# Kernel optimization log

Hardware: AMD Instinct MI355X
Metric: run time of the kernel (lower is better)

The kernel has to match this reference:

```python
import jax, jax.numpy as jnp
import numpy as np

N_NODES = 100000
IN_FEAT, HID, OUT_FEAT, GRID = 128, 64, 40, 8
N_EDGES = 1600000


def spmm(row, col, w, x):
    # out[i] = sum_{e: row[e]==i} w[e] * x[col[e]]
    return jax.ops.segment_sum(w[:, None] * x[col], row, num_segments=N_NODES)


def kan_layer(x, coeff):
    # coeff: [2, out, in, grid]; Fourier KAN: y[b,j] = sum_{i,k} cos(k x_bi) C0[j,i,k] + sin(k x_bi) C1[j,i,k]
    grid = coeff.shape[-1]
    k = jnp.arange(1, grid + 1, dtype=x.dtype)  # [G]
    ang = x[:, :, None] * k  # [N, in, G]
    y = jnp.einsum('bik,jik->bj', jnp.cos(ang), coeff[0])
    y = y + jnp.einsum('bik,jik->bj', jnp.sin(ang), coeff[1])
    return y


def setup_inputs() -> dict:
    key = jax.random.key(0)
    ks = jax.random.split(key, 8)
    scale = 1.0 / (np.sqrt(HID) * np.sqrt(GRID))
    return {
        'x': jax.random.normal(ks[0], (N_NODES, IN_FEAT), dtype=jnp.float32),
        'edge_row': jax.random.randint(ks[1], (N_EDGES,), 0, N_NODES),
        'edge_col': jax.random.randint(ks[2], (N_EDGES,), 0, N_NODES),
        'edge_weight': jax.random.uniform(ks[3], (N_EDGES,), dtype=jnp.float32),
        'W_in': jax.random.normal(ks[4], (IN_FEAT, HID), dtype=jnp.float32) / np.sqrt(IN_FEAT),
        'b_in': jnp.zeros((HID,), dtype=jnp.float32),
        'coeffs1': jax.random.normal(ks[5], (2, HID, HID, GRID), dtype=jnp.float32) * scale,
        'coeffs2': jax.random.normal(ks[6], (2, HID, HID, GRID), dtype=jnp.float32) * scale,
        'W_out': jax.random.normal(ks[7], (HID, OUT_FEAT), dtype=jnp.float32) / np.sqrt(HID),
    }


def reference(x, edge_row, edge_col, edge_weight, W_in, b_in, coeffs1, coeffs2, W_out):
    h = x @ W_in + b_in                                  # lin_in
    h = kan_layer(spmm(edge_row, edge_col, edge_weight, h), coeffs1)
    h = kan_layer(spmm(edge_row, edge_col, edge_weight, h), coeffs2)
    out = h @ W_out                                      # final bias-free linear
    return jax.nn.log_softmax(out, axis=-1)
```

## Files before the change

### kernel.cpp

```cpp
#include <hip/hip_runtime.h>
#include <hip/hip_bf16.h>
#include <string.h>


#define N_NODES 100000
#define IN_FEAT 128
#define HID 64
#define OUT_FEAT 40
#define NGRID 8
#define N_EDGES 1600000
#define NELEM (N_NODES * HID)

#define NB 98
#define CAP 18432
#define BCHUNK 4096
#define BIN_BLOCKS ((N_EDGES + BCHUNK - 1) / BCHUNK)

using short8 = __attribute__((ext_vector_type(8))) short;
using floatx4 = __attribute__((ext_vector_type(4))) float;
using uintx4 = __attribute__((ext_vector_type(4))) unsigned;

#define GLOAD_LDS16(gp, lp)                                                   \
  __builtin_amdgcn_global_load_lds(                                           \
      (const __attribute__((address_space(1))) unsigned*)(gp),                \
      (__attribute__((address_space(3))) unsigned*)(lp), 16, 0, 0)

__device__ __forceinline__ unsigned pack_bf16x2(float c, float s) {
  unsigned uc = __float_as_uint(c);
  unsigned us = __float_as_uint(s);
  uc += 0x7fffu + ((uc >> 16) & 1u);
  us += 0x7fffu + ((us >> 16) & 1u);
  return (uc >> 16) | (us & 0xffff0000u);
}

__device__ __forceinline__ unsigned cvtpk_bf16x2(float c, float s) {
  __hip_bfloat162 p = __float22bfloat162_rn(make_float2(c, s));
  unsigned r;
  memcpy(&r, &p, 4);
  return r;
}

__global__ __launch_bounds__(256) void lin_in_kernel(
    const float* __restrict__ x, const float* __restrict__ W,
    const float* __restrict__ b, float* __restrict__ h) {
  __shared__ __align__(16) float xs[16 * IN_FEAT];
  int t = threadIdx.x;
  int nb = blockIdx.x;
  const float4* xsrc = (const float4*)(x + (size_t)nb * 16 * IN_FEAT);
  float4* xd = (float4*)xs;
  xd[t] = xsrc[t];
  xd[t + 256] = xsrc[t + 256];
  __syncthreads();
  int lane = t & 63, wv = t >> 6;
  float bj = b[lane];
  float a0 = bj, a1 = bj, a2 = bj, a3 = bj;
  const float* xr = xs + wv * 4 * IN_FEAT;
  const float* Wj = W + lane;
#pragma unroll 4
  for (int i4 = 0; i4 < 32; i4++) {
    float4 x0 = *(const float4*)(xr + 0 * IN_FEAT + i4 * 4);
    float4 x1 = *(const float4*)(xr + 1 * IN_FEAT + i4 * 4);
    float4 x2 = *(const float4*)(xr + 2 * IN_FEAT + i4 * 4);
    float4 x3 = *(const float4*)(xr + 3 * IN_FEAT + i4 * 4);
    float w0 = Wj[(i4 * 4 + 0) * HID];
    float w1 = Wj[(i4 * 4 + 1) * HID];
    float w2 = Wj[(i4 * 4 + 2) * HID];
    float w3 = Wj[(i4 * 4 + 3) * HID];
    a0 = fmaf(x0.x, w0, a0); a0 = fmaf(x0.y, w1, a0); a0 = fmaf(x0.z, w2, a0); a0 = fmaf(x0.w, w3, a0);
    a1 = fmaf(x1.x, w0, a1); a1 = fmaf(x1.y, w1, a1); a1 = fmaf(x1.z, w2, a1); a1 = fmaf(x1.w, w3, a1);
    a2 = fmaf(x2.x, w0, a2); a2 = fmaf(x2.y, w1, a2); a2 = fmaf(x2.z, w2, a2); a2 = fmaf(x2.w, w3, a2);
    a3 = fmaf(x3.x, w0, a3); a3 = fmaf(x3.y, w1, a3); a3 = fmaf(x3.z, w2, a3); a3 = fmaf(x3.w, w3, a3);
  }
  size_t nbase = (size_t)nb * 16 + wv * 4;
  h[(nbase + 0) * HID + lane] = a0;
  h[(nbase + 1) * HID + lane] = a1;
  h[(nbase + 2) * HID + lane] = a2;
  h[(nbase + 3) * HID + lane] = a3;
}

__global__ __launch_bounds__(128) void binit_kernel(int* __restrict__ btail) {
  int t = threadIdx.x;
  if (t < NB) btail[t] = t * CAP;
}

__global__ __launch_bounds__(256) void bin_kernel(
    const int* __restrict__ row, const int* __restrict__ col,
    const float* __restrict__ w, int* __restrict__ btail,
    uint2* __restrict__ pack1) {
  __shared__ __align__(16) uint2 stage[BCHUNK];
  __shared__ int bcnt[NB];
  __shared__ int lbase[NB];
  __shared__ int gbase[NB];
  __shared__ int lcur[NB];
  __shared__ int sc[128];
  int t = threadIdx.x;
  int e0 = blockIdx.x * BCHUNK;
  if (t < NB) bcnt[t] = 0;
  __syncthreads();
  int rloc[16];
#pragma unroll
  for (int q = 0; q < 16; q++) {
    int e = e0 + q * 256 + t;
    int r = (e < N_EDGES) ? row[e] : -1;
    rloc[q] = r;
    if (r >= 0) atomicAdd(&bcnt[r >> 10], 1);
  }
  __syncthreads();
  int c = (t < NB) ? bcnt[t] : 0;
  if (t < 128) sc[t] = c;
  __syncthreads();
  int v = c;
#pragma unroll
  for (int off = 1; off < 128; off <<= 1) {
    int add = (t >= off && t < 128) ? sc[t - off] : 0;
    __syncthreads();
    if (t < 128) sc[t] = v = v + add;
    __syncthreads();
  }
  if (t < NB) {
    lbase[t] = v - c;
    lcur[t] = v - c;
    gbase[t] = atomicAdd(&btail[t], c);
  }
  __syncthreads();
#pragma unroll
  for (int q = 0; q < 16; q++) {
    int e = e0 + q * 256 + t;
    int r = rloc[q];
    if (r >= 0) {
      int p = atomicAdd(&lcur[r >> 10], 1);
      unsigned key = ((unsigned)(r & 1023) << 17) | (unsigned)col[e];
      stage[p] = make_uint2(key, __float_as_uint(w[e]));
    }
  }
  __syncthreads();
  int wv = t >> 6, lane = t & 63;
  for (int b = wv; b < NB; b += 4) {
    int len = bcnt[b], src = lbase[b];
    uint2* dst = pack1 + (size_t)gbase[b];
    for (int i = lane; i < len; i += 64)
      dst[i] = stage[src + i];
  }
}

__global__ __launch_bounds__(256) void bucket_finalize_kernel(
    const int* __restrict__ btail, const uint2* __restrict__ pack1,
    int* __restrict__ rowptr, uint2* __restrict__ pack2) {
  __shared__ int rcnt[1024];
  __shared__ int sc[256];
  __shared__ int binfo[2];
  int b = blockIdx.x, t = threadIdx.x;
  if (t < NB) sc[t] = btail[t] - t * CAP;
  rcnt[t] = 0; rcnt[t + 256] = 0; rcnt[t + 512] = 0; rcnt[t + 768] = 0;
  __syncthreads();
  if (t == 0) {
    int base = 0;
    for (int i = 0; i < b; i++) base += sc[i];
    binfo[0] = base;
    binfo[1] = sc[b];
  }
  __syncthreads();
  int base = binfo[0], len = binfo[1];
  const uint2* rec = pack1 + (size_t)b * CAP;
  for (int i = t; i < len; i += 256)
    atomicAdd(&rcnt[rec[i].x >> 17], 1);
  __syncthreads();
  int c0 = rcnt[4 * t], c1 = rcnt[4 * t + 1], c2 = rcnt[4 * t + 2], c3 = rcnt[4 * t + 3];
  int s4 = c0 + c1 + c2 + c3;
  sc[t] = s4;
  __syncthreads();
  int v = s4;
#pragma unroll
  for (int off = 1; off < 256; off <<= 1) {
    int add = (t >= off) ? sc[t - off] : 0;
    __syncthreads();
    sc[t] = v = v + add;
    __syncthreads();
  }
  int excl = v - s4;
  int p0 = base + excl;
  int p1 = p0 + c0, p2 = p1 + c1, p3 = p2 + c2;
  int r0 = (b << 10) + 4 * t;
  if (r0 + 0 < N_NODES) rowptr[r0 + 0] = p0;
  if (r0 + 1 < N_NODES) rowptr[r0 + 1] = p1;
  if (r0 + 2 < N_NODES) rowptr[r0 + 2] = p2;
  if (r0 + 3 < N_NODES) rowptr[r0 + 3] = p3;
  rcnt[4 * t] = p0; rcnt[4 * t + 1] = p1; rcnt[4 * t + 2] = p2; rcnt[4 * t + 3] = p3;
  __syncthreads();
  for (int i = t; i < len; i += 256) {
    uint2 p = rec[i];
    int pos = atomicAdd(&rcnt[p.x >> 17], 1);
    pack2[pos] = make_uint2(p.x & 0x1FFFFu, p.y);
  }
  if (b == NB - 1 && t == 0) rowptr[N_NODES] = N_EDGES;
}

__global__ __launch_bounds__(256) void repack_kernel(
    const float* __restrict__ coeffs, unsigned* __restrict__ Brep) {
  int idx = blockIdx.x * 256 + threadIdx.x;
  int ch = idx >> 13;
  int rem = idx & 8191;
  int blk = rem >> 8;
  int jt = blk >> 3, ks = blk & 7;
  int rem2 = rem & 255;
  int ls = rem2 >> 2;
  int quad = ls >> 4, m_n = ls & 15;
  int jj = rem2 & 3;
  int j = jt * 16 + m_n;
  int r = ks >> 1, km1 = ((ks & 1) << 2) | jj;
  int i = ch * 16 + quad * 4 + r;
  int ws = i * 8 + km1;
  float c0 = coeffs[(size_t)j * 512 + ws];
  float c1 = coeffs[32768 + (size_t)j * 512 + ws];
  Brep[idx] = pack_bf16x2(c0, c1);
}

template <int DO_FINAL>
__global__ __launch_bounds__(256, 4) void fused_spmm_kan_kernel(
    const int* __restrict__ rowptr, const uint2* __restrict__ pack,
    const float* __restrict__ hin, const unsigned* __restrict__ Brep,
    float* __restrict__ outp, const float* __restrict__ Wout) {
  __shared__ __align__(16) unsigned Bs[2][2048];
  __shared__ __align__(16) float s_tile[64 * 64];
  int t = threadIdx.x;
  int lane = t & 63, wv = t >> 6;
  int nb = blockIdx.x;
  const char* Gb = (const char*)Brep;

#pragma unroll
  for (int i = 0; i < 2; i++) {
    int c = wv + 4 * i;
    GLOAD_LDS16(Gb + c * 1024 + lane * 16, (char*)&Bs[0][0] + c * 1024);
  }

  {
    int rpi = nb * 64 + wv * 16 + lane;
    int rp = 0;
    if (lane < 17) rp = rowptr[rpi < N_NODES ? rpi : N_NODES];
    int slot = lane >> 4, f4 = lane & 15;
    const float4* h4 = (const float4*)hin;
    const unsigned long long* packq = (const unsigned long long*)pack;
    for (int i = 0; i < 16; i++) {
      int beg = __shfl(rp, i), end = __shfl(rp, i + 1);
      float4 v = make_float4(0.f, 0.f, 0.f, 0.f);
      for (int e = beg; e < end; e += 16) {
        int i0 = e + slot, i1 = i0 + 4, i2 = i0 + 8, i3 = i0 + 12;
        int c0 = i0 < end ? i0 : end - 1;
        int c1 = i1 < end ? i1 : end - 1;
        int c2 = i2 < end ? i2 : end - 1;
        int c3 = i3 < end ? i3 : end - 1;
        unsigned long long p0 = __builtin_nontemporal_load(packq + c0);
        unsigned long long p1 = __builtin_nontemporal_load(packq + c1);
        unsigned long long p2 = __builtin_nontemporal_load(packq + c2);
        unsigned long long p3 = __builtin_nontemporal_load(packq + c3);
        float4 h0 = h4[(size_t)(unsigned)p0 * 16 + f4];
        float4 h1 = h4[(size_t)(unsigned)p1 * 16 + f4];
        float4 h2 = h4[(size_t)(unsigned)p2 * 16 + f4];
        float4 h3 = h4[(size_t)(unsigned)p3 * 16 + f4];
        float w0 = (i0 < end) ? __uint_as_float((unsigned)(p0 >> 32)) : 0.f;
        float w1 = (i1 < end) ? __uint_as_float((unsigned)(p1 >> 32)) : 0.f;
        float w2 = (i2 < end) ? __uint_as_float((unsigned)(p2 >> 32)) : 0.f;
        float w3 = (i3 < end) ? __uint_as_float((unsigned)(p3 >> 32)) : 0.f;
        v.x = fmaf(w0, h0.x, v.x); v.y = fmaf(w0, h0.y, v.y);
        v.z = fmaf(w0, h0.z, v.z); v.w = fmaf(w0, h0.w, v.w);
        v.x = fmaf(w1, h1.x, v.x); v.y = fmaf(w1, h1.y, v.y);
        v.z = fmaf(w1, h1.z, v.z); v.w = fmaf(w1, h1.w, v.w);
        v.x = fmaf(w2, h2.x, v.x); v.y = fmaf(w2, h2.y, v.y);
        v.z = fmaf(w2, h2.z, v.z); v.w = fmaf(w2, h2.w, v.w);
        v.x = fmaf(w3, h3.x, v.x); v.y = fmaf(w3, h3.y, v.y);
        v.z = fmaf(w3, h3.z, v.z); v.w = fmaf(w3, h3.w, v.w);
      }
#pragma unroll
      for (int off = 16; off < 64; off <<= 1) {
        v.x += __shfl_xor(v.x, off);
        v.y += __shfl_xor(v.y, off);
        v.z += __shfl_xor(v.z, off);
        v.w += __shfl_xor(v.w, off);
      }
      if (slot == 0)
        *(float4*)&s_tile[(wv * 16 + i) * 64 + f4 * 4] = v;
    }
  }
  __syncthreads();

  int m_n = lane & 15, quad = lane >> 4;
  int node_sub = wv * 16 + m_n;
  float4 sv[4];
#pragma unroll
  for (int ch = 0; ch < 4; ch++)
    sv[ch] = *(const float4*)&s_tile[node_sub * 64 + ch * 16 + quad * 4];

  floatx4 acc[4];
#pragma unroll
  for (int jt = 0; jt < 4; jt++) acc[jt] = (floatx4){0.f, 0.f, 0.f, 0.f};
  short8 afr[8];

#pragma unroll
  for (int q = 0; q < 16; q++) {
    asm volatile("s_waitcnt vmcnt(0)" ::: "memory");
    __syncthreads();
    if (q < 15) {
      int qq = q + 1;
      const char* gsrc = Gb + (qq >> 2) * 32768 + (qq & 3) * 8192;
      char* ldst = (char*)&Bs[qq & 1][0];
#pragma unroll
      for (int i = 0; i < 2; i++) {
        int c = wv + 4 * i;
        GLOAD_LDS16(gsrc + c * 1024 + lane * 16, ldst + c * 1024);
      }
    }
    if ((q & 3) == 0) {
      int ch = q >> 2;
      float ss[4] = {sv[ch].x, sv[ch].y, sv[ch].z, sv[ch].w};
#pragma unroll
      for (int r = 0; r < 4; r++) {
        float s1, c1;
        __sincosf(ss[r], &s1, &c1);
        float ck = c1, sk = s1;
        unsigned wbuf[8];
#pragma unroll
        for (int km1 = 0; km1 < 8; km1++) {
          wbuf[km1] = cvtpk_bf16x2(ck, sk);
          float cn = fmaf(ck, c1, -sk * s1);
          float sn = fmaf(sk, c1, ck * s1);
          ck = cn; sk = sn;
        }
        uintx4 lo = (uintx4){wbuf[0], wbuf[1], wbuf[2], wbuf[3]};
        uintx4 hi = (uintx4){wbuf[4], wbuf[5], wbuf[6], wbuf[7]};
        memcpy(&afr[2 * r], &lo, 16);
        memcpy(&afr[2 * r + 1], &hi, 16);
      }
    }
    const char* Bb = (const char*)&Bs[q & 1][0];
    int jt = q & 3;
#pragma unroll
    for (int ks = 0; ks < 8; ks++) {
      short8 bf = *reinterpret_cast<const short8*>(Bb + ks * 1024 + lane * 16);
      acc[jt] = __builtin_amdgcn_mfma_f32_16x16x32_bf16(afr[ks], bf, acc[jt], 0, 0, 0);
    }
  }

  if (DO_FINAL == 0) {
#pragma unroll
    for (int jt = 0; jt < 4; jt++) {
#pragma unroll
      for (int reg = 0; reg < 4; reg++) {
        int node = nb * 64 + wv * 16 + quad * 4 + reg;
        if (node < N_NODES)
          outp[(size_t)node * HID + jt * 16 + m_n] = acc[jt][reg];
      }
    }
  } else {
#pragma unroll
    for (int jt = 0; jt < 4; jt++) {
#pragma unroll
      for (int reg = 0; reg < 4; reg++)
        s_tile[(wv * 16 + quad * 4 + reg) * 64 + jt * 16 + m_n] = acc[jt][reg];
    }
    __syncthreads();
    bool jvalid = lane < OUT_FEAT;
    int jc = jvalid ? lane : 0;
    float wl[HID];
#pragma unroll
    for (int i2 = 0; i2 < HID; i2++)
      wl[i2] = Wout[i2 * OUT_FEAT + jc];
    int nwbase = nb * 64 + wv * 16;
    for (int ns = 0; ns < 16; ns += 2) {
      const float* h0p = &s_tile[(wv * 16 + ns) * 64];
      const float* h1p = h0p + 64;
      float d0 = 0.f, d1 = 0.f;
#pragma unroll
      for (int i4 = 0; i4 < 16; i4++) {
        float4 a = *(const float4*)(h0p + i4 * 4);
        float4 b = *(const float4*)(h1p + i4 * 4);
        d0 = fmaf(a.x, wl[i4 * 4 + 0], d0);  d1 = fmaf(b.x, wl[i4 * 4 + 0], d1);
        d0 = fmaf(a.y, wl[i4 * 4 + 1], d0);  d1 = fmaf(b.y, wl[i4 * 4 + 1], d1);
        d0 = fmaf(a.z, wl[i4 * 4 + 2], d0);  d1 = fmaf(b.z, wl[i4 * 4 + 2], d1);
        d0 = fmaf(a.w, wl[i4 * 4 + 3], d0);  d1 = fmaf(b.w, wl[i4 * 4 + 3], d1);
      }
      float m0 = jvalid ? d0 : -1e30f;
      float m1 = jvalid ? d1 : -1e30f;
#pragma unroll
      for (int off = 32; off; off >>= 1) {
        m0 = fmaxf(m0, __shfl_xor(m0, off));
        m1 = fmaxf(m1, __shfl_xor(m1, off));
      }
      float e0 = jvalid ? expf(d0 - m0) : 0.f;
      float e1 = jvalid ? expf(d1 - m1) : 0.f;
      float s0 = e0, s1 = e1;
#pragma unroll
      for (int off = 32; off; off >>= 1) {
        s0 += __shfl_xor(s0, off);
        s1 += __shfl_xor(s1, off);
      }
      float l0 = m0 + logf(s0);
      float l1 = m1 + logf(s1);
      int n0 = nwbase + ns, n1 = n0 + 1;
      if (jvalid) {
        if (n0 < N_NODES) outp[(size_t)n0 * OUT_FEAT + lane] = d0 - l0;
        if (n1 < N_NODES) outp[(size_t)n1 * OUT_FEAT + lane] = d1 - l1;
      }
    }
  }
}

extern "C" void kernel_launch(void* const* d_in, const int* in_sizes, int n_in,
                              void* d_out, int out_size, void* d_ws, size_t ws_size,
                              hipStream_t stream) {
  (void)in_sizes; (void)n_in; (void)out_size; (void)ws_size;
  const float* x    = (const float*)d_in[0];
  const int*   erow = (const int*)d_in[1];
  const int*   ecol = (const int*)d_in[2];
  const float* ew   = (const float*)d_in[3];
  const float* W_in = (const float*)d_in[4];
  const float* b_in = (const float*)d_in[5];
  const float* c1   = (const float*)d_in[6];
  const float* c2   = (const float*)d_in[7];
  const float* Wout = (const float*)d_in[8];
  float* out = (float*)d_out;

  float* h0 = (float*)d_ws;
  float* h1 = h0 + NELEM;

  unsigned* xw     = (unsigned*)(void*)x;
  unsigned* Brep1  = xw;
  unsigned* Brep2  = xw + 32768;
  int*      btail  = (int*)(xw + 65536);
  int*      rowptr = (int*)(xw + 66048);
  uint2*    pack1  = (uint2*)(xw + 262144);
  uint2*    pack2  = (uint2*)(xw + 3932160);

  const int fgrid = (N_NODES + 63) / 64;

  lin_in_kernel<<<N_NODES / 16, 256, 0, stream>>>(x, W_in, b_in, h0);

  repack_kernel<<<128, 256, 0, stream>>>(c1, Brep1);
  repack_kernel<<<128, 256, 0, stream>>>(c2, Brep2);

  binit_kernel<<<1, 128, 0, stream>>>(btail);
  bin_kernel<<<BIN_BLOCKS, 256, 0, stream>>>(erow, ecol, ew, btail, pack1);
  bucket_finalize_kernel<<<NB, 256, 0, stream>>>(btail, pack1, rowptr, pack2);

  fused_spmm_kan_kernel<0><<<fgrid, 256, 0, stream>>>(
      rowptr, pack2, h0, Brep1, h1, nullptr);
  fused_spmm_kan_kernel<1><<<fgrid, 256, 0, stream>>>(
      rowptr, pack2, h1, Brep2, out, Wout);
}
```

Measured before the change: 425.4 us.

## Merge prep kernels and make fused SpMM-KAN kernels persistent with atomic tile queue

The input linear layer, both coefficient repacks and the bucket-tail init are folded into one prep kernel that dispatches on block index. The prep kernel also resets two tile counters. The two fused SpMM+KAN kernels now launch a fixed grid of 1280 blocks, and each block pulls 64-node tiles from an atomic counter until all are done. This cuts launch overhead and evens out load across tiles with uneven row degrees, at the cost of an atomic plus a barrier per tile and a grid size tuned by hand.

```diff
diff --git a/kernel.cpp b/kernel.cpp
--- a/kernel.cpp
+++ b/kernel.cpp
@@ -15,6 +15,8 @@
 #define CAP 18432
 #define BCHUNK 4096
 #define BIN_BLOCKS ((N_EDGES + BCHUNK - 1) / BCHUNK)
+#define NTILES ((N_NODES + 63) / 64)
+#define FGRID 1280
 
 using short8 = __attribute__((ext_vector_type(8))) short;
 using floatx4 = __attribute__((ext_vector_type(4))) float;
@@ -40,47 +42,70 @@
   return r;
 }
 
-__global__ __launch_bounds__(256) void lin_in_kernel(
+__global__ __launch_bounds__(256) void prep_kernel(
     const float* __restrict__ x, const float* __restrict__ W,
-    const float* __restrict__ b, float* __restrict__ h) {
+    const float* __restrict__ b, float* __restrict__ h,
+    const float* __restrict__ c1, const float* __restrict__ c2,
+    unsigned* __restrict__ Brep1, unsigned* __restrict__ Brep2,
+    int* __restrict__ btail, int* __restrict__ ctrs) {
   __shared__ __align__(16) float xs[16 * IN_FEAT];
   int t = threadIdx.x;
   int nb = blockIdx.x;
-  const float4* xsrc = (const float4*)(x + (size_t)nb * 16 * IN_FEAT);
-  float4* xd = (float4*)xs;
-  xd[t] = xsrc[t];
-  xd[t + 256] = xsrc[t + 256];
-  __syncthreads();
-  int lane = t & 63, wv = t >> 6;
-  float bj = b[lane];
-  float a0 = bj, a1 = bj, a2 = bj, a3 = bj;
-  const float* xr = xs + wv * 4 * IN_FEAT;
-  const float* Wj = W + lane;
+  if (nb < 6250) {
+    const float4* xsrc = (const float4*)(x + (size_t)nb * 16 * IN_FEAT);
+    float4* xd = (float4*)xs;
+    xd[t] = xsrc[t];
+    xd[t + 256] = xsrc[t + 256];
+    __syncthreads();
+    int lane = t & 63, wv = t >> 6;
+    float bj = b[lane];
+    float a0 = bj, a1 = bj, a2 = bj, a3 = bj;
+    const float* xr = xs + wv * 4 * IN_FEAT;
+    const float* Wj = W + lane;
 #pragma unroll 4
-  for (int i4 = 0; i4 < 32; i4++) {
-    float4 x0 = *(const float4*)(xr + 0 * IN_FEAT + i4 * 4);
-    float4 x1 = *(const float4*)(xr + 1 * IN_FEAT + i4 * 4);
-    float4 x2 = *(const float4*)(xr + 2 * IN_FEAT + i4 * 4);
-    float4 x3 = *(const float4*)(xr + 3 * IN_FEAT + i4 * 4);
-    float w0 = Wj[(i4 * 4 + 0) * HID];
-    float w1 = Wj[(i4 * 4 + 1) * HID];
-    float w2 = Wj[(i4 * 4 + 2) * HID];
-    float w3 = Wj[(i4 * 4 + 3) * HID];
-    a0 = fmaf(x0.x, w0, a0); a0 = fmaf(x0.y, w1, a0); a0 = fmaf(x0.z, w2, a0); a0 = fmaf(x0.w, w3, a0);
-    a1 = fmaf(x1.x, w0, a1); a1 = fmaf(x1.y, w1, a1); a1 = fmaf(x1.z, w2, a1); a1 = fmaf(x1.w, w3, a1);
-    a2 = fmaf(x2.x, w0, a2); a2 = fmaf(x2.y, w1, a2); a2 = fmaf(x2.z, w2, a2); a2 = fmaf(x2.w, w3, a2);
-    a3 = fmaf(x3.x, w0, a3); a3 = fmaf(x3.y, w1, a3); a3 = fmaf(x3.z, w2, a3); a3 = fmaf(x3.w, w3, a3);
-  }
-  size_t nbase = (size_t)nb * 16 + wv * 4;
-  h[(nbase + 0) * HID + lane] = a0;
-  h[(nbase + 1) * HID + lane] = a1;
-  h[(nbase + 2) * HID + lane] = a2;
-  h[(nbase + 3) * HID + lane] = a3;
-}
-
-__global__ __launch_bounds__(128) void binit_kernel(int* __restrict__ btail) {
-  int t = threadIdx.x;
-  if (t < NB) btail[t] = t * CAP;
+    for (int i4 = 0; i4 < 32; i4++) {
+      float4 x0 = *(const float4*)(xr + 0 * IN_FEAT + i4 * 4);
+      float4 x1 = *(const float4*)(xr + 1 * IN_FEAT + i4 * 4);
+      float4 x2 = *(const float4*)(xr + 2 * IN_FEAT + i4 * 4);
+      float4 x3 = *(const float4*)(xr + 3 * IN_FEAT + i4 * 4);
+      float w0 = Wj[(i4 * 4 + 0) * HID];
+      float w1 = Wj[(i4 * 4 + 1) * HID];
+      float w2 = Wj[(i4 * 4 + 2) * HID];
+      float w3 = Wj[(i4 * 4 + 3) * HID];
+      a0 = fmaf(x0.x, w0, a0); a0 = fmaf(x0.y, w1, a0); a0 = fmaf(x0.z, w2, a0); a0 = fmaf(x0.w, w3, a0);
+      a1 = fmaf(x1.x, w0, a1); a1 = fmaf(x1.y, w1, a1); a1 = fmaf(x1.z, w2, a1); a1 = fmaf(x1.w, w3, a1);
+      a2 = fmaf(x2.x, w0, a2); a2 = fmaf(x2.y, w1, a2); a2 = fmaf(x2.z, w2, a2); a2 = fmaf(x2.w, w3, a2);
+      a3 = fmaf(x3.x, w0, a3); a3 = fmaf(x3.y, w1, a3); a3 = fmaf(x3.z, w2, a3); a3 = fmaf(x3.w, w3, a3);
+    }
+    size_t nbase = (size_t)nb * 16 + wv * 4;
+    h[(nbase + 0) * HID + lane] = a0;
+    h[(nbase + 1) * HID + lane] = a1;
+    h[(nbase + 2) * HID + lane] = a2;
+    h[(nbase + 3) * HID + lane] = a3;
+  } else if (nb < 6506) {
+    int rb = nb - 6250;
+    const float* coeffs = (rb < 128) ? c1 : c2;
+    unsigned* Brep = (rb < 128) ? Brep1 : Brep2;
+    int idx = (rb & 127) * 256 + t;
+    int ch = idx >> 13;
+    int rem = idx & 8191;
+    int blk = rem >> 8;
+    int jt = blk >> 3, ks = blk & 7;
+    int rem2 = rem & 255;
+    int ls = rem2 >> 2;
+    int quad = ls >> 4, m_n = ls & 15;
+    int jj = rem2 & 3;
+    int j = jt * 16 + m_n;
+    int r = ks >> 1, km1 = ((ks & 1) << 2) | jj;
+    int i = ch * 16 + quad * 4 + r;
+    int ws = i * 8 + km1;
+    float cc0 = coeffs[(size_t)j * 512 + ws];
+    float cc1 = coeffs[32768 + (size_t)j * 512 + ws];
+    Brep[idx] = pack_bf16x2(cc0, cc1);
+  } else {
+    if (t < NB) btail[t] = t * CAP;
+    if (t == 128) { ctrs[0] = 0; ctrs[1] = 0; }
+  }
 }
 
 __global__ __launch_bounds__(256) void bin_kernel(
@@ -195,210 +220,197 @@
   if (b == NB - 1 && t == 0) rowptr[N_NODES] = N_EDGES;
 }
 
-__global__ __launch_bounds__(256) void repack_kernel(
-    const float* __restrict__ coeffs, unsigned* __restrict__ Brep) {
-  int idx = blockIdx.x * 256 + threadIdx.x;
-  int ch = idx >> 13;
-  int rem = idx & 8191;
-  int blk = rem >> 8;
-  int jt = blk >> 3, ks = blk & 7;
-  int rem2 = rem & 255;
-  int ls = rem2 >> 2;
-  int quad = ls >> 4, m_n = ls & 15;
-  int jj = rem2 & 3;
-  int j = jt * 16 + m_n;
-  int r = ks >> 1, km1 = ((ks & 1) << 2) | jj;
-  int i = ch * 16 + quad * 4 + r;
-  int ws = i * 8 + km1;
-  float c0 = coeffs[(size_t)j * 512 + ws];
-  float c1 = coeffs[32768 + (size_t)j * 512 + ws];
-  Brep[idx] = pack_bf16x2(c0, c1);
-}
-
 template <int DO_FINAL>
 __global__ __launch_bounds__(256, 4) void fused_spmm_kan_kernel(
     const int* __restrict__ rowptr, const uint2* __restrict__ pack,
     const float* __restrict__ hin, const unsigned* __restrict__ Brep,
-    float* __restrict__ outp, const float* __restrict__ Wout) {
+    float* __restrict__ outp, const float* __restrict__ Wout,
+    int* __restrict__ ctr) {
   __shared__ __align__(16) unsigned Bs[2][2048];
   __shared__ __align__(16) float s_tile[64 * 64];
+  __shared__ int tile_sm;
   int t = threadIdx.x;
   int lane = t & 63, wv = t >> 6;
-  int nb = blockIdx.x;
   const char* Gb = (const char*)Brep;
-
-#pragma unroll
-  for (int i = 0; i < 2; i++) {
-    int c = wv + 4 * i;
-    GLOAD_LDS16(Gb + c * 1024 + lane * 16, (char*)&Bs[0][0] + c * 1024);
-  }
-
-  {
-    int rpi = nb * 64 + wv * 16 + lane;
-    int rp = 0;
-    if (lane < 17) rp = rowptr[rpi < N_NODES ? rpi : N_NODES];
-    int slot = lane >> 4, f4 = lane & 15;
-    const float4* h4 = (const float4*)hin;
-    const unsigned long long* packq = (const unsigned long long*)pack;
-    for (int i = 0; i < 16; i++) {
-      int beg = __shfl(rp, i), end = __shfl(rp, i + 1);
-      float4 v = make_float4(0.f, 0.f, 0.f, 0.f);
-      for (int e = beg; e < end; e += 16) {
-        int i0 = e + slot, i1 = i0 + 4, i2 = i0 + 8, i3 = i0 + 12;
-        int c0 = i0 < end ? i0 : end - 1;
-        int c1 = i1 < end ? i1 : end - 1;
-        int c2 = i2 < end ? i2 : end - 1;
-        int c3 = i3 < end ? i3 : end - 1;
-        unsigned long long p0 = __builtin_nontemporal_load(packq + c0);
-        unsigned long long p1 = __builtin_nontemporal_load(packq + c1);
-        unsigned long long p2 = __builtin_nontemporal_load(packq + c2);
-        unsigned long long p3 = __builtin_nontemporal_load(packq + c3);
-        float4 h0 = h4[(size_t)(unsigned)p0 * 16 + f4];
-        float4 h1 = h4[(size_t)(unsigned)p1 * 16 + f4];
-        float4 h2 = h4[(size_t)(unsigned)p2 * 16 + f4];
-        float4 h3 = h4[(size_t)(unsigned)p3 * 16 + f4];
-        float w0 = (i0 < end) ? __uint_as_float((unsigned)(p0 >> 32)) : 0.f;
-        float w1 = (i1 < end) ? __uint_as_float((unsigned)(p1 >> 32)) : 0.f;
-        float w2 = (i2 < end) ? __uint_as_float((unsigned)(p2 >> 32)) : 0.f;
-        float w3 = (i3 < end) ? __uint_as_float((unsigned)(p3 >> 32)) : 0.f;
-        v.x = fmaf(w0, h0.x, v.x); v.y = fmaf(w0, h0.y, v.y);
-        v.z = fmaf(w0, h0.z, v.z); v.w = fmaf(w0, h0.w, v.w);
-        v.x = fmaf(w1, h1.x, v.x); v.y = fmaf(w1, h1.y, v.y);
-        v.z = fmaf(w1, h1.z, v.z); v.w = fmaf(w1, h1.w, v.w);
-        v.x = fmaf(w2, h2.x, v.x); v.y = fmaf(w2, h2.y, v.y);
-        v.z = fmaf(w2, h2.z, v.z); v.w = fmaf(w2, h2.w, v.w);
-        v.x = fmaf(w3, h3.x, v.x); v.y = fmaf(w3, h3.y, v.y);
-        v.z = fmaf(w3, h3.z, v.z); v.w = fmaf(w3, h3.w, v.w);
-      }
-#pragma unroll
-      for (int off = 16; off < 64; off <<= 1) {
-        v.x += __shfl_xor(v.x, off);
-        v.y += __shfl_xor(v.y, off);
-        v.z += __shfl_xor(v.z, off);
-        v.w += __shfl_xor(v.w, off);
-      }
-      if (slot == 0)
-        *(float4*)&s_tile[(wv * 16 + i) * 64 + f4 * 4] = v;
-    }
-  }
-  __syncthreads();
-
   int m_n = lane & 15, quad = lane >> 4;
-  int node_sub = wv * 16 + m_n;
-  float4 sv[4];
-#pragma unroll
-  for (int ch = 0; ch < 4; ch++)
-    sv[ch] = *(const float4*)&s_tile[node_sub * 64 + ch * 16 + quad * 4];
-
-  floatx4 acc[4];
-#pragma unroll
-  for (int jt = 0; jt < 4; jt++) acc[jt] = (floatx4){0.f, 0.f, 0.f, 0.f};
-  short8 afr[8];
-
-#pragma unroll
-  for (int q = 0; q < 16; q++) {
-    asm volatile("s_waitcnt vmcnt(0)" ::: "memory");
-    __syncthreads();
-    if (q < 15) {
-      int qq = q + 1;
-      const char* gsrc = Gb + (qq >> 2) * 32768 + (qq & 3) * 8192;
-      char* ldst = (char*)&Bs[qq & 1][0];
-#pragma unroll
-      for (int i = 0; i < 2; i++) {
-        int c = wv + 4 * i;
-        GLOAD_LDS16(gsrc + c * 1024 + lane * 16, ldst + c * 1024);
-      }
-    }
-    if ((q & 3) == 0) {
-      int ch = q >> 2;
-      float ss[4] = {sv[ch].x, sv[ch].y, sv[ch].z, sv[ch].w};
-#pragma unroll
-      for (int r = 0; r < 4; r++) {
-        float s1, c1;
-        __sincosf(ss[r], &s1, &c1);
-        float ck = c1, sk = s1;
-        unsigned wbuf[8];
-#pragma unroll
-        for (int km1 = 0; km1 < 8; km1++) {
-          wbuf[km1] = cvtpk_bf16x2(ck, sk);
-          float cn = fmaf(ck, c1, -sk * s1);
-          float sn = fmaf(sk, c1, ck * s1);
-          ck = cn; sk = sn;
-        }
-        uintx4 lo = (uintx4){wbuf[0], wbuf[1], wbuf[2], wbuf[3]};
-        uintx4 hi = (uintx4){wbuf[4], wbuf[5], wbuf[6], wbuf[7]};
-        memcpy(&afr[2 * r], &lo, 16);
-        memcpy(&afr[2 * r + 1], &hi, 16);
-      }
-    }
-    const char* Bb = (const char*)&Bs[q & 1][0];
-    int jt = q & 3;
-#pragma unroll
-    for (int ks = 0; ks < 8; ks++) {
-      short8 bf = *reinterpret_cast<const short8*>(Bb + ks * 1024 + lane * 16);
-      acc[jt] = __builtin_amdgcn_mfma_f32_16x16x32_bf16(afr[ks], bf, acc[jt], 0, 0, 0);
-    }
-  }
-
-  if (DO_FINAL == 0) {
-#pragma unroll
-    for (int jt = 0; jt < 4; jt++) {
-#pragma unroll
-      for (int reg = 0; reg < 4; reg++) {
-        int node = nb * 64 + wv * 16 + quad * 4 + reg;
-        if (node < N_NODES)
-          outp[(size_t)node * HID + jt * 16 + m_n] = acc[jt][reg];
-      }
-    }
-  } else {
-#pragma unroll
-    for (int jt = 0; jt < 4; jt++) {
-#pragma unroll
-      for (int reg = 0; reg < 4; reg++)
-        s_tile[(wv * 16 + quad * 4 + reg) * 64 + jt * 16 + m_n] = acc[jt][reg];
-    }
-    __syncthreads();
-    bool jvalid = lane < OUT_FEAT;
-    int jc = jvalid ? lane : 0;
-    float wl[HID];
-#pragma unroll
-    for (int i2 = 0; i2 < HID; i2++)
-      wl[i2] = Wout[i2 * OUT_FEAT + jc];
-    int nwbase = nb * 64 + wv * 16;
-    for (int ns = 0; ns < 16; ns += 2) {
-      const float* h0p = &s_tile[(wv * 16 + ns) * 64];
-      const float* h1p = h0p + 64;
-      float d0 = 0.f, d1 = 0.f;
-#pragma unroll
-      for (int i4 = 0; i4 < 16; i4++) {
-        float4 a = *(const float4*)(h0p + i4 * 4);
-        float4 b = *(const float4*)(h1p + i4 * 4);
-        d0 = fmaf(a.x, wl[i4 * 4 + 0], d0);  d1 = fmaf(b.x, wl[i4 * 4 + 0], d1);
-        d0 = fmaf(a.y, wl[i4 * 4 + 1], d0);  d1 = fmaf(b.y, wl[i4 * 4 + 1], d1);
-        d0 = fmaf(a.z, wl[i4 * 4 + 2], d0);  d1 = fmaf(b.z, wl[i4 * 4 + 2], d1);
-        d0 = fmaf(a.w, wl[i4 * 4 + 3], d0);  d1 = fmaf(b.w, wl[i4 * 4 + 3], d1);
-      }
-      float m0 = jvalid ? d0 : -1e30f;
-      float m1 = jvalid ? d1 : -1e30f;
-#pragma unroll
-      for (int off = 32; off; off >>= 1) {
-        m0 = fmaxf(m0, __shfl_xor(m0, off));
-        m1 = fmaxf(m1, __shfl_xor(m1, off));
-      }
-      float e0 = jvalid ? expf(d0 - m0) : 0.f;
-      float e1 = jvalid ? expf(d1 - m1) : 0.f;
-      float s0 = e0, s1 = e1;
-#pragma unroll
-      for (int off = 32; off; off >>= 1) {
-        s0 += __shfl_xor(s0, off);
-        s1 += __shfl_xor(s1, off);
-      }
-      float l0 = m0 + logf(s0);
-      float l1 = m1 + logf(s1);
-      int n0 = nwbase + ns, n1 = n0 + 1;
-      if (jvalid) {
-        if (n0 < N_NODES) outp[(size_t)n0 * OUT_FEAT + lane] = d0 - l0;
-        if (n1 < N_NODES) outp[(size_t)n1 * OUT_FEAT + lane] = d1 - l1;
+
+  while (true) {
+    if (t == 0) tile_sm = atomicAdd(ctr, 1);
+    __syncthreads();
+    int nb = tile_sm;
+    if (nb >= NTILES) break;
+
+#pragma unroll
+    for (int i = 0; i < 2; i++) {
+      int c = wv + 4 * i;
+      GLOAD_LDS16(Gb + c * 1024 + lane * 16, (char*)&Bs[0][0] + c * 1024);
+    }
+
+    {
+      int rpi = nb * 64 + wv * 16 + lane;
+      int rp = 0;
+      if (lane < 17) rp = rowptr[rpi < N_NODES ? rpi : N_NODES];
+      int slot = lane >> 4, f4 = lane & 15;
+      const float4* h4 = (const float4*)hin;
+      const unsigned long long* packq = (const unsigned long long*)pack;
+      for (int i = 0; i < 16; i++) {
+        int beg = __shfl(rp, i), end = __shfl(rp, i + 1);
+        float4 v = make_float4(0.f, 0.f, 0.f, 0.f);
+        for (int e = beg; e < end; e += 16) {
+          int i0 = e + slot, i1 = i0 + 4, i2 = i0 + 8, i3 = i0 + 12;
+          int c0 = i0 < end ? i0 : end - 1;
+          int c1 = i1 < end ? i1 : end - 1;
+          int c2 = i2 < end ? i2 : end - 1;
+          int c3 = i3 < end ? i3 : end - 1;
+          unsigned long long p0 = __builtin_nontemporal_load(packq + c0);
+          unsigned long long p1 = __builtin_nontemporal_load(packq + c1);
+          unsigned long long p2 = __builtin_nontemporal_load(packq + c2);
+          unsigned long long p3 = __builtin_nontemporal_load(packq + c3);
+          float4 h0 = h4[(size_t)(unsigned)p0 * 16 + f4];
+          float4 h1 = h4[(size_t)(unsigned)p1 * 16 + f4];
+          float4 h2 = h4[(size_t)(unsigned)p2 * 16 + f4];
+          float4 h3 = h4[(size_t)(unsigned)p3 * 16 + f4];
+          float w0 = (i0 < end) ? __uint_as_float((unsigned)(p0 >> 32)) : 0.f;
+          float w1 = (i1 < end) ? __uint_as_float((unsigned)(p1 >> 32)) : 0.f;
+          float w2 = (i2 < end) ? __uint_as_float((unsigned)(p2 >> 32)) : 0.f;
+          float w3 = (i3 < end) ? __uint_as_float((unsigned)(p3 >> 32)) : 0.f;
+          v.x = fmaf(w0, h0.x, v.x); v.y = fmaf(w0, h0.y, v.y);
+          v.z = fmaf(w0, h0.z, v.z); v.w = fmaf(w0, h0.w, v.w);
+          v.x = fmaf(w1, h1.x, v.x); v.y = fmaf(w1, h1.y, v.y);
+          v.z = fmaf(w1, h1.z, v.z); v.w = fmaf(w1, h1.w, v.w);
+          v.x = fmaf(w2, h2.x, v.x); v.y = fmaf(w2, h2.y, v.y);
+          v.z = fmaf(w2, h2.z, v.z); v.w = fmaf(w2, h2.w, v.w);
+          v.x = fmaf(w3, h3.x, v.x); v.y = fmaf(w3, h3.y, v.y);
+          v.z = fmaf(w3, h3.z, v.z); v.w = fmaf(w3, h3.w, v.w);
+        }
+#pragma unroll
+        for (int off = 16; off < 64; off <<= 1) {
+          v.x += __shfl_xor(v.x, off);
+          v.y += __shfl_xor(v.y, off);
+          v.z += __shfl_xor(v.z, off);
+          v.w += __shfl_xor(v.w, off);
+        }
+        if (slot == 0)
+          *(float4*)&s_tile[(wv * 16 + i) * 64 + f4 * 4] = v;
+      }
+    }
+    __syncthreads();
+
+    float4 sv[4];
+#pragma unroll
+    for (int ch = 0; ch < 4; ch++)
+      sv[ch] = *(const float4*)&s_tile[(wv * 16 + m_n) * 64 + ch * 16 + quad * 4];
+
+    floatx4 acc[4];
+#pragma unroll
+    for (int jt = 0; jt < 4; jt++) acc[jt] = (floatx4){0.f, 0.f, 0.f, 0.f};
+    short8 afr[8];
+
+#pragma unroll
+    for (int q = 0; q < 16; q++) {
+      asm volatile("s_waitcnt vmcnt(0)" ::: "memory");
+      __syncthreads();
+      if (q < 15) {
+        int qq = q + 1;
+        const char* gsrc = Gb + (qq >> 2) * 32768 + (qq & 3) * 8192;
+        char* ldst = (char*)&Bs[qq & 1][0];
+#pragma unroll
+        for (int i = 0; i < 2; i++) {
+          int c = wv + 4 * i;
+          GLOAD_LDS16(gsrc + c * 1024 + lane * 16, ldst + c * 1024);
+        }
+      }
+      if ((q & 3) == 0) {
+        int ch = q >> 2;
+        float ss[4] = {sv[ch].x, sv[ch].y, sv[ch].z, sv[ch].w};
+#pragma unroll
+        for (int r = 0; r < 4; r++) {
+          float s1, c1;
+          __sincosf(ss[r], &s1, &c1);
+          float ck = c1, sk = s1;
+          unsigned wbuf[8];
+#pragma unroll
+          for (int km1 = 0; km1 < 8; km1++) {
+            wbuf[km1] = cvtpk_bf16x2(ck, sk);
+            float cn = fmaf(ck, c1, -sk * s1);
+            float sn = fmaf(sk, c1, ck * s1);
+            ck = cn; sk = sn;
+          }
+          uintx4 lo = (uintx4){wbuf[0], wbuf[1], wbuf[2], wbuf[3]};
+          uintx4 hi = (uintx4){wbuf[4], wbuf[5], wbuf[6], wbuf[7]};
+          memcpy(&afr[2 * r], &lo, 16);
+          memcpy(&afr[2 * r + 1], &hi, 16);
+        }
+      }
+      const char* Bb = (const char*)&Bs[q & 1][0];
+      int jt = q & 3;
+#pragma unroll
+      for (int ks = 0; ks < 8; ks++) {
+        short8 bf = *reinterpret_cast<const short8*>(Bb + ks * 1024 + lane * 16);
+        acc[jt] = __builtin_amdgcn_mfma_f32_16x16x32_bf16(afr[ks], bf, acc[jt], 0, 0, 0);
+      }
+    }
+
+    if (DO_FINAL == 0) {
+#pragma unroll
+      for (int jt = 0; jt < 4; jt++) {
+#pragma unroll
+        for (int reg = 0; reg < 4; reg++) {
+          int node = nb * 64 + wv * 16 + quad * 4 + reg;
+          if (node < N_NODES)
+            outp[(size_t)node * HID + jt * 16 + m_n] = acc[jt][reg];
+        }
+      }
+    } else {
+#pragma unroll
+      for (int jt = 0; jt < 4; jt++) {
+#pragma unroll
+        for (int reg = 0; reg < 4; reg++)
+          s_tile[(wv * 16 + quad * 4 + reg) * 64 + jt * 16 + m_n] = acc[jt][reg];
+      }
+      __syncthreads();
+      bool jvalid = lane < OUT_FEAT;
+      int jc = jvalid ? lane : 0;
+      float wl[HID];
+#pragma unroll
+      for (int i2 = 0; i2 < HID; i2++)
+        wl[i2] = Wout[i2 * OUT_FEAT + jc];
+      int nwbase = nb * 64 + wv * 16;
+      for (int ns = 0; ns < 16; ns += 2) {
+        const float* h0p = &s_tile[(wv * 16 + ns) * 64];
+        const float* h1p = h0p + 64;
+        float d0 = 0.f, d1 = 0.f;
+#pragma unroll
+        for (int i4 = 0; i4 < 16; i4++) {
+          float4 a = *(const float4*)(h0p + i4 * 4);
+          float4 b = *(const float4*)(h1p + i4 * 4);
+          d0 = fmaf(a.x, wl[i4 * 4 + 0], d0);  d1 = fmaf(b.x, wl[i4 * 4 + 0], d1);
+          d0 = fmaf(a.y, wl[i4 * 4 + 1], d0);  d1 = fmaf(b.y, wl[i4 * 4 + 1], d1);
+          d0 = fmaf(a.z, wl[i4 * 4 + 2], d0);  d1 = fmaf(b.z, wl[i4 * 4 + 2], d1);
+          d0 = fmaf(a.w, wl[i4 * 4 + 3], d0);  d1 = fmaf(b.w, wl[i4 * 4 + 3], d1);
+        }
+        float m0 = jvalid ? d0 : -1e30f;
+        float m1 = jvalid ? d1 : -1e30f;
+#pragma unroll
+        for (int off = 32; off; off >>= 1) {
+          m0 = fmaxf(m0, __shfl_xor(m0, off));
+          m1 = fmaxf(m1, __shfl_xor(m1, off));
+        }
+        float e0 = jvalid ? expf(d0 - m0) : 0.f;
+        float e1 = jvalid ? expf(d1 - m1) : 0.f;
+        float s0 = e0, s1 = e1;
+#pragma unroll
+        for (int off = 32; off; off >>= 1) {
+          s0 += __shfl_xor(s0, off);
+          s1 += __shfl_xor(s1, off);
+        }
+        float l0 = m0 + logf(s0);
+        float l1 = m1 + logf(s1);
+        int n0 = nwbase + ns, n1 = n0 + 1;
+        if (jvalid) {
+          if (n0 < N_NODES) outp[(size_t)n0 * OUT_FEAT + lane] = d0 - l0;
+          if (n1 < N_NODES) outp[(size_t)n1 * OUT_FEAT + lane] = d1 - l1;
+        }
       }
     }
   }
@@ -426,23 +438,18 @@
   unsigned* Brep1  = xw;
   unsigned* Brep2  = xw + 32768;
   int*      btail  = (int*)(xw + 65536);
+  int*      ctrs   = (int*)(xw + 65792);
   int*      rowptr = (int*)(xw + 66048);
   uint2*    pack1  = (uint2*)(xw + 262144);
   uint2*    pack2  = (uint2*)(xw + 3932160);
 
-  const int fgrid = (N_NODES + 63) / 64;
-
-  lin_in_kernel<<<N_NODES / 16, 256, 0, stream>>>(x, W_in, b_in, h0);
-
-  repack_kernel<<<128, 256, 0, stream>>>(c1, Brep1);
-  repack_kernel<<<128, 256, 0, stream>>>(c2, Brep2);
-
-  binit_kernel<<<1, 128, 0, stream>>>(btail);
+  prep_kernel<<<6507, 256, 0, stream>>>(x, W_in, b_in, h0, c1, c2,
+                                        Brep1, Brep2, btail, ctrs);
   bin_kernel<<<BIN_BLOCKS, 256, 0, stream>>>(erow, ecol, ew, btail, pack1);
   bucket_finalize_kernel<<<NB, 256, 0, stream>>>(btail, pack1, rowptr, pack2);
 
-  fused_spmm_kan_kernel<0><<<fgrid, 256, 0, stream>>>(
-      rowptr, pack2, h0, Brep1, h1, nullptr);
-  fused_spmm_kan_kernel<1><<<fgrid, 256, 0, stream>>>(
-      rowptr, pack2, h1, Brep2, out, Wout);
-}
+  fused_spmm_kan_kernel<0><<<FGRID, 256, 0, stream>>>(
+      rowptr, pack2, h0, Brep1, h1, nullptr, ctrs + 0);
+  fused_spmm_kan_kernel<1><<<FGRID, 256, 0, stream>>>(
+      rowptr, pack2, h1, Brep2, out, Wout, ctrs + 1);
+}
```

After: 517.8 us. 21.7% more time.
